# Kernel optimization log

Hardware: AMD Instinct MI355X
Metric: run time of the kernel (lower is better)

Reference implementation:

```python
import jax, jax.numpy as jnp
import numpy as np

N = 20000          # num nodes
E_EDGES = 160000   # num edges
D = 128            # input feature dim
H = 128            # hidden dim
C = 128            # num_classes (expert output dim)
NE = 4             # num_experts
COEF = 0.01        # load-balancing loss coefficient


def setup_inputs() -> dict:
    key = jax.random.key(0)
    ks = jax.random.split(key, 8)
    x = jax.random.normal(ks[0], (N, D), jnp.float32)
    edge_index = jax.random.randint(ks[1], (2, E_EDGES), 0, N)
    x_agg = jax.random.normal(ks[2], (N, D), jnp.float32)
    # gate params (w_gate is zeros-init in source; use small randn so gating is exercised)
    w_gate = jax.random.normal(ks[3], (D, NE), jnp.float32) * 0.1
    gate_threshold = jax.random.normal(ks[4], (NE,), jnp.float32) * 0.1
    experts_mask = jnp.ones((NE,), jnp.float32)
    # per-expert 2-layer GCN weights (vectorized over expert dim)
    W1 = jax.random.normal(ks[5], (NE, D, H), jnp.float32) * (1.0 / np.sqrt(D))
    b1 = jnp.zeros((NE, H), jnp.float32)
    W2 = jax.random.normal(ks[6], (NE, H, C), jnp.float32) * (1.0 / np.sqrt(H))
    b2 = jnp.zeros((NE, C), jnp.float32)
    return {"x": x, "edge_index": edge_index, "x_agg": x_agg,
            "w_gate": w_gate, "gate_threshold": gate_threshold,
            "experts_mask": experts_mask, "W1": W1, "b1": b1, "W2": W2, "b2": b2}


def _gcn_norm(edge_index):
    src, dst = edge_index[0], edge_index[1]
    deg = jax.ops.segment_sum(jnp.ones((src.shape[0],), jnp.float32), dst, num_segments=N)
    deg = jnp.maximum(deg, 1.0)
    norm = jax.lax.rsqrt(deg[src] * deg[dst])  # symmetric GCN normalization per edge
    return src, dst, norm


def _agg(h, src, dst, norm):
    # h: [N, F] -> normalized neighbor sum: [N, F]
    return jax.ops.segment_sum(h[src] * norm[:, None], dst, num_segments=N)


def _ste_sign(s):
    # SAGMMGateBackward: sign in forward, identity in backward (straight-through)
    return s + jax.lax.stop_gradient(jnp.sign(s) - s)


def reference(x, edge_index, x_agg, w_gate, gate_threshold, experts_mask, W1, b1, W2, b2):
    src, dst, norm = _gcn_norm(edge_index)

    # --- noisy_top_any gating (eval path: no noise), add_sigmoid=True ---
    clean_logits = x_agg @ w_gate                       # [N, NE]
    gate_scores = jax.nn.sigmoid(clean_logits)          # [N, NE]
    # sign-based straight-through gate vs learned threshold, masked by experts_mask
    gates = jax.nn.relu(_ste_sign(gate_scores - gate_threshold[None, :]))
    gates = gates * experts_mask[None, :]               # [N, NE], binary in forward

    # --- experts: 4 two-layer GCNs, vectorized over the expert dim ---
    agg_x = _agg(x, src, dst, norm)                     # shared first aggregation [N, D]
    h = jax.nn.relu(jnp.einsum('nd,edh->enh', agg_x, W1) + b1[:, None, :])   # [NE, N, H]
    agg_h = jax.vmap(lambda hh: _agg(hh, src, dst, norm))(h)                 # [NE, N, H]
    expert_out = jnp.einsum('enh,ehc->enc', agg_h, W2) + b2[:, None, :]      # [NE, N, C]

    # --- combine expert outputs with gates ---
    output = jnp.einsum('ne,enc->nc', gates, expert_out)                     # [N, C]

    # --- cv_squared load-balancing loss on per-expert importance ---
    importance = gates.sum(axis=0)                                           # [NE]
    load_loss = COEF * (jnp.var(importance) / (jnp.mean(importance) ** 2 + 1e-10))
    return output, load_loss
```

## Files before the change

### kernel.cpp

```cpp
#include <hip/hip_runtime.h>
#include <cstdint>
#include <cstddef>

#define NNODES 20000
#define NEDGES 160000
#define DFEAT  128
#define NEXP   4

typedef unsigned short u16;
typedef __attribute__((ext_vector_type(8))) short short8v;
typedef __attribute__((ext_vector_type(4))) float float4v;

static __device__ __forceinline__ u16 f2bf(float f) {
    union { float f; unsigned int i; } v; v.f = f;
    unsigned int r = (v.i + 0x7FFFu + ((v.i >> 16) & 1u)) >> 16;
    return (u16)r;
}
static __device__ __forceinline__ float lo2f(unsigned int u) { return __uint_as_float(u << 16); }
static __device__ __forceinline__ float hi2f(unsigned int u) { return __uint_as_float(u & 0xFFFF0000u); }


__global__ void k_pre(const int* __restrict__ ei,
                      const float* __restrict__ W1, const float* __restrict__ W2,
                      const float* __restrict__ x_agg, const float* __restrict__ w_gate,
                      const float* __restrict__ thr, const float* __restrict__ mask,
                      float* __restrict__ deg, u16* __restrict__ W1t, u16* __restrict__ W2t,
                      float* __restrict__ gates, float* __restrict__ importance) {
    int b = blockIdx.x;
    if (b < 625) {
        int e = b * 256 + threadIdx.x;
        if (e < NEDGES) atomicAdd(&deg[ei[NEDGES + e]], 1.0f);
        return;
    }
    if (b < 1137) {
        int gid = (b - 625) * 256 + threadIdx.x;
        int arr = gid >> 16;
        int rem = gid & 65535;
        int e = rem >> 14;
        int cw = rem & 16383;
        int c = cw >> 7, k = cw & 127;
        const float* W = arr ? W2 : W1;
        u16* Wt = arr ? W2t : W1t;
        Wt[rem] = f2bf(W[(size_t)e * 16384 + (size_t)k * 128 + c]);
        return;
    }
    int n = (b - 1137) * 256 + threadIdx.x;
    float4 lg = make_float4(0.f, 0.f, 0.f, 0.f);
    if (n < NNODES) {
        const float4* xr = (const float4*)(x_agg + (size_t)n * DFEAT);
        const float4* wg = (const float4*)w_gate;
        for (int k4 = 0; k4 < 32; ++k4) {
            float4 xv = xr[k4];
            float4 w0 = wg[4 * k4 + 0], w1 = wg[4 * k4 + 1];
            float4 w2 = wg[4 * k4 + 2], w3 = wg[4 * k4 + 3];
            lg.x += xv.x * w0.x + xv.y * w1.x + xv.z * w2.x + xv.w * w3.x;
            lg.y += xv.x * w0.y + xv.y * w1.y + xv.z * w2.y + xv.w * w3.y;
            lg.z += xv.x * w0.z + xv.y * w1.z + xv.z * w2.z + xv.w * w3.z;
            lg.w += xv.x * w0.w + xv.y * w1.w + xv.z * w2.w + xv.w * w3.w;
        }
    }
    float g[4];
    float lv[4] = {lg.x, lg.y, lg.z, lg.w};
    for (int e = 0; e < 4; ++e) {
        float sgm = 1.0f / (1.0f + expf(-lv[e]));
        g[e] = (sgm - thr[e] > 0.0f) ? mask[e] : 0.0f;
        if (n >= NNODES) g[e] = 0.0f;
    }
    if (n < NNODES) ((float4*)gates)[n] = make_float4(g[0], g[1], g[2], g[3]);
    int lane = threadIdx.x & 63;
    for (int e = 0; e < 4; ++e) {
        float v = g[e];
        for (int off = 32; off >= 1; off >>= 1) v += __shfl_down(v, off);
        if (lane == 0) atomicAdd(&importance[e], v);
    }
}

__global__ void k_scan(const float* __restrict__ deg, int* __restrict__ rowstart) {
    __shared__ int part[1024];
    int t = threadIdx.x;
    const int PER = 20;
    int base = t * PER;
    int s = 0;
    for (int i = 0; i < PER; ++i) {
        int n = base + i;
        if (n < NNODES) s += (int)deg[n];
    }
    part[t] = s;
    __syncthreads();
    for (int off = 1; off < 1024; off <<= 1) {
        int v = (t >= off) ? part[t - off] : 0;
        __syncthreads();
        part[t] += v;
        __syncthreads();
    }
    int run = part[t] - s;
    for (int i = 0; i < PER; ++i) {
        int n = base + i;
        if (n < NNODES) {
            rowstart[n] = run;
            run += (int)deg[n];
        }
    }
    if (t == 1023) rowstart[NNODES] = part[1023];
}

__global__ void k_fill(const int* __restrict__ ei, const float* __restrict__ deg,
                       const int* __restrict__ rowstart, int* __restrict__ cursor,
                       int* __restrict__ csrc, float* __restrict__ cnrm) {
    int e = blockIdx.x * 256 + threadIdx.x;
    if (e >= NEDGES) return;
    int s = ei[e], d = ei[NEDGES + e];
    int pos = atomicAdd(&cursor[d], 1);
    int slot = rowstart[d] + pos;
    csrc[slot] = s;
    float ds = fmaxf(deg[s], 1.0f), dd = fmaxf(deg[d], 1.0f);
    cnrm[slot] = 1.0f / sqrtf(ds * dd);
}

__global__ void k_aggx(const float* __restrict__ x, const int* __restrict__ rowstart,
                       const int* __restrict__ csrc, const float* __restrict__ cnrm,
                       u16* __restrict__ aggx) {
    int gid = blockIdx.x * 256 + threadIdx.x;
    if (gid >= NNODES * 32) return;
    int c4 = gid & 31, node = gid >> 5;
    int r0 = rowstart[node], r1 = rowstart[node + 1];
    float ax = 0.f, ay = 0.f, az = 0.f, aw = 0.f;
    for (int j = r0; j < r1; ++j) {
        int s = csrc[j];
        float wv = cnrm[j];
        float4 v = ((const float4*)(x + (size_t)s * DFEAT))[c4];
        ax += wv * v.x; ay += wv * v.y; az += wv * v.z; aw += wv * v.w;
    }
    uint2 o;
    o.x = ((unsigned)f2bf(ay) << 16) | f2bf(ax);
    o.y = ((unsigned)f2bf(aw) << 16) | f2bf(az);
    ((uint2*)(aggx + (size_t)node * DFEAT))[c4] = o;
}

__launch_bounds__(320)
__global__ void k_gemm1(const u16* __restrict__ aggx, const u16* __restrict__ W1t,
                        const float* __restrict__ b1, u16* __restrict__ h) {
    int e = blockIdx.y;
    int w = threadIdx.x >> 6, l = threadIdx.x & 63;
    int rbase = blockIdx.x * 80 + w * 16;
    int lr = l & 15, kg = l >> 4;

    const short8v* A8 = (const short8v*)aggx;
    const short8v* B8 = (const short8v*)(W1t + (size_t)e * 16384);

    short8v a[4];
#pragma unroll
    for (int kk = 0; kk < 4; ++kk) a[kk] = A8[(size_t)(rbase + lr) * 16 + kk * 4 + kg];

    u16* hb = h + (size_t)e * NNODES * DFEAT;
#pragma unroll
    for (int c = 0; c < 8; ++c) {
        float4v acc = {0.f, 0.f, 0.f, 0.f};
#pragma unroll
        for (int kk = 0; kk < 4; ++kk) {
            short8v b = B8[(c * 16 + lr) * 16 + kk * 4 + kg];
            acc = __builtin_amdgcn_mfma_f32_16x16x32_bf16(a[kk], b, acc, 0, 0, 0);
        }
        float bv = b1[e * DFEAT + c * 16 + lr];
#pragma unroll
        for (int i = 0; i < 4; ++i) {
            int node = rbase + kg * 4 + i;
            float vv = fmaxf(acc[i] + bv, 0.f);
            hb[(size_t)node * DFEAT + c * 16 + lr] = f2bf(vv);
        }
    }
}

__global__ void k_aggh(const u16* __restrict__ h, const int* __restrict__ rowstart,
                       const int* __restrict__ csrc, const float* __restrict__ cnrm,
                       const float* __restrict__ gates, u16* __restrict__ aggh) {
    int gid = blockIdx.x * 256 + threadIdx.x;
    if (gid >= NEXP * NNODES * 16) return;
    int l8 = gid & 15;
    int ni = gid >> 4;
    int node = ni % NNODES;
    int e = ni / NNODES;
    if (gates[(size_t)node * 4 + e] == 0.0f) return;
    const u16* hb = h + (size_t)e * NNODES * DFEAT;
    int r0 = rowstart[node], r1 = rowstart[node + 1];
    float a0 = 0.f, a1 = 0.f, a2 = 0.f, a3 = 0.f, a4 = 0.f, a5 = 0.f, a6 = 0.f, a7 = 0.f;
    for (int j = r0; j < r1; ++j) {
        int s = csrc[j];
        float wv = cnrm[j];
        uint4 v = ((const uint4*)(hb + (size_t)s * DFEAT))[l8];
        a0 += wv * lo2f(v.x); a1 += wv * hi2f(v.x);
        a2 += wv * lo2f(v.y); a3 += wv * hi2f(v.y);
        a4 += wv * lo2f(v.z); a5 += wv * hi2f(v.z);
        a6 += wv * lo2f(v.w); a7 += wv * hi2f(v.w);
    }
    uint4 o;
    o.x = ((unsigned)f2bf(a1) << 16) | f2bf(a0);
    o.y = ((unsigned)f2bf(a3) << 16) | f2bf(a2);
    o.z = ((unsigned)f2bf(a5) << 16) | f2bf(a4);
    o.w = ((unsigned)f2bf(a7) << 16) | f2bf(a6);
    ((uint4*)(aggh + (size_t)ni * DFEAT))[l8] = o;
}

__launch_bounds__(320)
__global__ void k_gemm2(const u16* __restrict__ aggh, const u16* __restrict__ W2t,
                        const float* __restrict__ b2, const float* __restrict__ gates,
                        const float* __restrict__ importance, float* __restrict__ out) {
    if (blockIdx.x == 0 && blockIdx.y == 0 && threadIdx.x == 0) {
        float v0 = importance[0], v1 = importance[1], v2 = importance[2], v3 = importance[3];
        float mean = 0.25f * (v0 + v1 + v2 + v3);
        float d0 = v0 - mean, d1 = v1 - mean, d2 = v2 - mean, d3 = v3 - mean;
        float var = 0.25f * (d0 * d0 + d1 * d1 + d2 * d2 + d3 * d3);
        out[(size_t)NNODES * DFEAT] = 0.01f * var / (mean * mean + 1e-10f);
    }
    int w = threadIdx.x >> 6, l = threadIdx.x & 63;
    int rbase = blockIdx.x * 80 + w * 16;
    int cb = blockIdx.y * 2;
    int lr = l & 15, kg = l >> 4;

    float4v acc[2];
    acc[0] = (float4v){0.f, 0.f, 0.f, 0.f};
    acc[1] = (float4v){0.f, 0.f, 0.f, 0.f};

#pragma unroll
    for (int e = 0; e < NEXP; ++e) {
        const short8v* A8 = (const short8v*)(aggh + (size_t)e * NNODES * DFEAT);
        const short8v* B8 = (const short8v*)(W2t + (size_t)e * 16384);
        short8v a[4];
#pragma unroll
        for (int kk = 0; kk < 4; ++kk) a[kk] = A8[(size_t)(rbase + lr) * 16 + kk * 4 + kg];
        float g[4];
#pragma unroll
        for (int i = 0; i < 4; ++i) g[i] = gates[(size_t)(rbase + kg * 4 + i) * 4 + e];
#pragma unroll
        for (int c = 0; c < 2; ++c) {
            float4v t = {0.f, 0.f, 0.f, 0.f};
#pragma unroll
            for (int kk = 0; kk < 4; ++kk) {
                short8v b = B8[((cb + c) * 16 + lr) * 16 + kk * 4 + kg];
                t = __builtin_amdgcn_mfma_f32_16x16x32_bf16(a[kk], b, t, 0, 0, 0);
            }
            float bv = b2[e * DFEAT + (cb + c) * 16 + lr];
#pragma unroll
            for (int i = 0; i < 4; ++i) acc[c][i] += g[i] * (t[i] + bv);
        }
    }

#pragma unroll
    for (int c = 0; c < 2; ++c)
#pragma unroll
        for (int i = 0; i < 4; ++i) {
            int node = rbase + kg * 4 + i;
            out[(size_t)node * DFEAT + (cb + c) * 16 + lr] = acc[c][i];
        }
}

extern "C" void kernel_launch(void* const* d_in, const int* in_sizes, int n_in,
                              void* d_out, int out_size, void* d_ws, size_t ws_size,
                              hipStream_t stream) {
    const float* x      = (const float*)d_in[0];
    const int*   ei     = (const int*)d_in[1];
    const float* x_agg  = (const float*)d_in[2];
    const float* w_gate = (const float*)d_in[3];
    const float* thr    = (const float*)d_in[4];
    const float* mask   = (const float*)d_in[5];
    const float* W1     = (const float*)d_in[6];
    const float* b1     = (const float*)d_in[7];
    const float* W2     = (const float*)d_in[8];
    const float* b2     = (const float*)d_in[9];
    float* out = (float*)d_out;
    float* ws  = (float*)d_ws;

    float* deg        = ws;
    int*   cursor     = (int*)(ws + 20000);
    float* importance = ws + 40000;
    int*   rowstart   = (int*)(ws + 40960);
    int*   csrc       = (int*)(ws + 61440);
    float* cnrm       = ws + 221440;
    float* gates      = ws + 381440;
    u16*   W1t        = (u16*)(ws + 461440);
    u16*   W2t        = (u16*)(ws + 494208);
    u16*   aggx       = (u16*)(ws + 526976);
    u16*   h          = (u16*)(ws + 1806976);
    u16*   aggh       = (u16*)(ws + 6926976);

    hipMemsetAsync(d_ws, 0, 40008 * sizeof(float), stream);

    k_pre<<<1216, 256, 0, stream>>>(ei, W1, W2, x_agg, w_gate, thr, mask,
                                    deg, W1t, W2t, gates, importance);
    k_scan<<<1, 1024, 0, stream>>>(deg, rowstart);
    k_fill<<<(NEDGES + 255) / 256, 256, 0, stream>>>(ei, deg, rowstart, cursor, csrc, cnrm);
    k_aggx<<<(NNODES * 32) / 256, 256, 0, stream>>>(x, rowstart, csrc, cnrm, aggx);
    k_gemm1<<<dim3(250, NEXP), 320, 0, stream>>>(aggx, W1t, b1, h);
    k_aggh<<<(NEXP * NNODES * 16) / 256, 256, 0, stream>>>(h, rowstart, csrc, cnrm, gates, aggh);
    k_gemm2<<<dim3(250, 4), 320, 0, stream>>>(aggh, W2t, b2, gates, importance, out);
}
```

Measured before the change: 258.8 us.

## Pre-convert x to bf16, unroll gather loops, tile weight transpose via LDS

Converts x to bf16 inside the preprocessing kernel so the first neighbor aggregation gathers half as many bytes per edge, with each thread handling 8 features instead of 4. Both aggregation kernels unroll the edge loop by four to keep more independent gathers in flight. The weight transpose now goes through a padded shared-memory tile so both its reads and writes are coalesced. This adds a full pass over x and extra workspace, and rounds x to bf16 before aggregation instead of after, which slightly changes numerics.

```diff
diff --git a/kernel.cpp b/kernel.cpp
--- a/kernel.cpp
+++ b/kernel.cpp
@@ -16,63 +16,98 @@
     unsigned int r = (v.i + 0x7FFFu + ((v.i >> 16) & 1u)) >> 16;
     return (u16)r;
 }
+static __device__ __forceinline__ unsigned pack2(float a, float b) {
+    return ((unsigned)f2bf(b) << 16) | f2bf(a);
+}
 static __device__ __forceinline__ float lo2f(unsigned int u) { return __uint_as_float(u << 16); }
 static __device__ __forceinline__ float hi2f(unsigned int u) { return __uint_as_float(u & 0xFFFF0000u); }
 
-
-__global__ void k_pre(const int* __restrict__ ei,
+static __device__ __forceinline__ void acc8(float w, uint4 v, float* a) {
+    a[0] += w * lo2f(v.x); a[1] += w * hi2f(v.x);
+    a[2] += w * lo2f(v.y); a[3] += w * hi2f(v.y);
+    a[4] += w * lo2f(v.z); a[5] += w * hi2f(v.z);
+    a[6] += w * lo2f(v.w); a[7] += w * hi2f(v.w);
+}
+
+
+__global__ void k_pre(const int* __restrict__ ei, const float* __restrict__ x,
                       const float* __restrict__ W1, const float* __restrict__ W2,
                       const float* __restrict__ x_agg, const float* __restrict__ w_gate,
                       const float* __restrict__ thr, const float* __restrict__ mask,
                       float* __restrict__ deg, u16* __restrict__ W1t, u16* __restrict__ W2t,
-                      float* __restrict__ gates, float* __restrict__ importance) {
+                      float* __restrict__ gates, float* __restrict__ importance,
+                      u16* __restrict__ xbf) {
     int b = blockIdx.x;
     if (b < 625) {
         int e = b * 256 + threadIdx.x;
         if (e < NEDGES) atomicAdd(&deg[ei[NEDGES + e]], 1.0f);
         return;
     }
-    if (b < 1137) {
-        int gid = (b - 625) * 256 + threadIdx.x;
-        int arr = gid >> 16;
-        int rem = gid & 65535;
-        int e = rem >> 14;
-        int cw = rem & 16383;
-        int c = cw >> 7, k = cw & 127;
+    if (b < 753) {
+        __shared__ u16 tile[32][33];
+        int tb = b - 625;
+        int arr = tb >> 6;
+        int t6 = tb & 63;
+        int e  = t6 >> 4;
+        int kt = (t6 >> 2) & 3;
+        int ct = t6 & 3;
         const float* W = arr ? W2 : W1;
         u16* Wt = arr ? W2t : W1t;
-        Wt[rem] = f2bf(W[(size_t)e * 16384 + (size_t)k * 128 + c]);
+        int ty = threadIdx.x >> 5, tx = threadIdx.x & 31;
+#pragma unroll
+        for (int r = 0; r < 4; ++r) {
+            int k = kt * 32 + ty + r * 8;
+            int c = ct * 32 + tx;
+            tile[ty + r * 8][tx] = f2bf(W[(size_t)e * 16384 + (size_t)k * 128 + c]);
+        }
+        __syncthreads();
+#pragma unroll
+        for (int r = 0; r < 4; ++r) {
+            int c = ct * 32 + ty + r * 8;
+            int k = kt * 32 + tx;
+            Wt[(size_t)e * 16384 + (size_t)c * 128 + k] = tile[tx][ty + r * 8];
+        }
         return;
     }
-    int n = (b - 1137) * 256 + threadIdx.x;
-    float4 lg = make_float4(0.f, 0.f, 0.f, 0.f);
-    if (n < NNODES) {
-        const float4* xr = (const float4*)(x_agg + (size_t)n * DFEAT);
-        const float4* wg = (const float4*)w_gate;
-        for (int k4 = 0; k4 < 32; ++k4) {
-            float4 xv = xr[k4];
-            float4 w0 = wg[4 * k4 + 0], w1 = wg[4 * k4 + 1];
-            float4 w2 = wg[4 * k4 + 2], w3 = wg[4 * k4 + 3];
-            lg.x += xv.x * w0.x + xv.y * w1.x + xv.z * w2.x + xv.w * w3.x;
-            lg.y += xv.x * w0.y + xv.y * w1.y + xv.z * w2.y + xv.w * w3.y;
-            lg.z += xv.x * w0.z + xv.y * w1.z + xv.z * w2.z + xv.w * w3.z;
-            lg.w += xv.x * w0.w + xv.y * w1.w + xv.z * w2.w + xv.w * w3.w;
-        }
-    }
-    float g[4];
-    float lv[4] = {lg.x, lg.y, lg.z, lg.w};
-    for (int e = 0; e < 4; ++e) {
-        float sgm = 1.0f / (1.0f + expf(-lv[e]));
-        g[e] = (sgm - thr[e] > 0.0f) ? mask[e] : 0.0f;
-        if (n >= NNODES) g[e] = 0.0f;
-    }
-    if (n < NNODES) ((float4*)gates)[n] = make_float4(g[0], g[1], g[2], g[3]);
-    int lane = threadIdx.x & 63;
-    for (int e = 0; e < 4; ++e) {
-        float v = g[e];
-        for (int off = 32; off >= 1; off >>= 1) v += __shfl_down(v, off);
-        if (lane == 0) atomicAdd(&importance[e], v);
-    }
+    if (b < 832) {
+        int n = (b - 753) * 256 + threadIdx.x;
+        float4 lg = make_float4(0.f, 0.f, 0.f, 0.f);
+        if (n < NNODES) {
+            const float4* xr = (const float4*)(x_agg + (size_t)n * DFEAT);
+            const float4* wg = (const float4*)w_gate;
+            for (int k4 = 0; k4 < 32; ++k4) {
+                float4 xv = xr[k4];
+                float4 w0 = wg[4 * k4 + 0], w1 = wg[4 * k4 + 1];
+                float4 w2 = wg[4 * k4 + 2], w3 = wg[4 * k4 + 3];
+                lg.x += xv.x * w0.x + xv.y * w1.x + xv.z * w2.x + xv.w * w3.x;
+                lg.y += xv.x * w0.y + xv.y * w1.y + xv.z * w2.y + xv.w * w3.y;
+                lg.z += xv.x * w0.z + xv.y * w1.z + xv.z * w2.z + xv.w * w3.z;
+                lg.w += xv.x * w0.w + xv.y * w1.w + xv.z * w2.w + xv.w * w3.w;
+            }
+        }
+        float g[4];
+        float lv[4] = {lg.x, lg.y, lg.z, lg.w};
+        for (int e = 0; e < 4; ++e) {
+            float sgm = 1.0f / (1.0f + expf(-lv[e]));
+            g[e] = (sgm - thr[e] > 0.0f) ? mask[e] : 0.0f;
+            if (n >= NNODES) g[e] = 0.0f;
+        }
+        if (n < NNODES) ((float4*)gates)[n] = make_float4(g[0], g[1], g[2], g[3]);
+        int lane = threadIdx.x & 63;
+        for (int e = 0; e < 4; ++e) {
+            float v = g[e];
+            for (int off = 32; off >= 1; off >>= 1) v += __shfl_down(v, off);
+            if (lane == 0) atomicAdd(&importance[e], v);
+        }
+        return;
+    }
+    int t8 = (b - 832) * 256 + threadIdx.x;
+    const float4* xr = (const float4*)x + (size_t)t8 * 2;
+    float4 v0 = xr[0], v1 = xr[1];
+    uint4 o;
+    o.x = pack2(v0.x, v0.y); o.y = pack2(v0.z, v0.w);
+    o.z = pack2(v1.x, v1.y); o.w = pack2(v1.z, v1.w);
+    ((uint4*)xbf)[t8] = o;
 }
 
 __global__ void k_scan(const float* __restrict__ deg, int* __restrict__ rowstart) {
@@ -117,24 +152,34 @@
     cnrm[slot] = 1.0f / sqrtf(ds * dd);
 }
 
-__global__ void k_aggx(const float* __restrict__ x, const int* __restrict__ rowstart,
+__global__ void k_aggx(const u16* __restrict__ xbf, const int* __restrict__ rowstart,
                        const int* __restrict__ csrc, const float* __restrict__ cnrm,
                        u16* __restrict__ aggx) {
     int gid = blockIdx.x * 256 + threadIdx.x;
-    if (gid >= NNODES * 32) return;
-    int c4 = gid & 31, node = gid >> 5;
+    if (gid >= NNODES * 16) return;
+    int l8 = gid & 15, node = gid >> 4;
     int r0 = rowstart[node], r1 = rowstart[node + 1];
-    float ax = 0.f, ay = 0.f, az = 0.f, aw = 0.f;
-    for (int j = r0; j < r1; ++j) {
+    float a[8] = {0.f, 0.f, 0.f, 0.f, 0.f, 0.f, 0.f, 0.f};
+    int j = r0;
+    for (; j + 4 <= r1; j += 4) {
+        int s0 = csrc[j], s1 = csrc[j + 1], s2 = csrc[j + 2], s3 = csrc[j + 3];
+        float w0 = cnrm[j], w1 = cnrm[j + 1], w2 = cnrm[j + 2], w3 = cnrm[j + 3];
+        uint4 v0 = ((const uint4*)(xbf + (size_t)s0 * DFEAT))[l8];
+        uint4 v1 = ((const uint4*)(xbf + (size_t)s1 * DFEAT))[l8];
+        uint4 v2 = ((const uint4*)(xbf + (size_t)s2 * DFEAT))[l8];
+        uint4 v3 = ((const uint4*)(xbf + (size_t)s3 * DFEAT))[l8];
+        acc8(w0, v0, a); acc8(w1, v1, a); acc8(w2, v2, a); acc8(w3, v3, a);
+    }
+    for (; j < r1; ++j) {
         int s = csrc[j];
-        float wv = cnrm[j];
-        float4 v = ((const float4*)(x + (size_t)s * DFEAT))[c4];
-        ax += wv * v.x; ay += wv * v.y; az += wv * v.z; aw += wv * v.w;
-    }
-    uint2 o;
-    o.x = ((unsigned)f2bf(ay) << 16) | f2bf(ax);
-    o.y = ((unsigned)f2bf(aw) << 16) | f2bf(az);
-    ((uint2*)(aggx + (size_t)node * DFEAT))[c4] = o;
+        float w = cnrm[j];
+        uint4 v = ((const uint4*)(xbf + (size_t)s * DFEAT))[l8];
+        acc8(w, v, a);
+    }
+    uint4 o;
+    o.x = pack2(a[0], a[1]); o.y = pack2(a[2], a[3]);
+    o.z = pack2(a[4], a[5]); o.w = pack2(a[6], a[7]);
+    ((uint4*)(aggx + (size_t)node * DFEAT))[l8] = o;
 }
 
 __launch_bounds__(320)
@@ -183,21 +228,26 @@
     if (gates[(size_t)node * 4 + e] == 0.0f) return;
     const u16* hb = h + (size_t)e * NNODES * DFEAT;
     int r0 = rowstart[node], r1 = rowstart[node + 1];
-    float a0 = 0.f, a1 = 0.f, a2 = 0.f, a3 = 0.f, a4 = 0.f, a5 = 0.f, a6 = 0.f, a7 = 0.f;
-    for (int j = r0; j < r1; ++j) {
+    float a[8] = {0.f, 0.f, 0.f, 0.f, 0.f, 0.f, 0.f, 0.f};
+    int j = r0;
+    for (; j + 4 <= r1; j += 4) {
+        int s0 = csrc[j], s1 = csrc[j + 1], s2 = csrc[j + 2], s3 = csrc[j + 3];
+        float w0 = cnrm[j], w1 = cnrm[j + 1], w2 = cnrm[j + 2], w3 = cnrm[j + 3];
+        uint4 v0 = ((const uint4*)(hb + (size_t)s0 * DFEAT))[l8];
+        uint4 v1 = ((const uint4*)(hb + (size_t)s1 * DFEAT))[l8];
+        uint4 v2 = ((const uint4*)(hb + (size_t)s2 * DFEAT))[l8];
+        uint4 v3 = ((const uint4*)(hb + (size_t)s3 * DFEAT))[l8];
+        acc8(w0, v0, a); acc8(w1, v1, a); acc8(w2, v2, a); acc8(w3, v3, a);
+    }
+    for (; j < r1; ++j) {
         int s = csrc[j];
-        float wv = cnrm[j];
+        float w = cnrm[j];
         uint4 v = ((const uint4*)(hb + (size_t)s * DFEAT))[l8];
-        a0 += wv * lo2f(v.x); a1 += wv * hi2f(v.x);
-        a2 += wv * lo2f(v.y); a3 += wv * hi2f(v.y);
-        a4 += wv * lo2f(v.z); a5 += wv * hi2f(v.z);
-        a6 += wv * lo2f(v.w); a7 += wv * hi2f(v.w);
+        acc8(w, v, a);
     }
     uint4 o;
-    o.x = ((unsigned)f2bf(a1) << 16) | f2bf(a0);
-    o.y = ((unsigned)f2bf(a3) << 16) | f2bf(a2);
-    o.z = ((unsigned)f2bf(a5) << 16) | f2bf(a4);
-    o.w = ((unsigned)f2bf(a7) << 16) | f2bf(a6);
+    o.x = pack2(a[0], a[1]); o.y = pack2(a[2], a[3]);
+    o.z = pack2(a[4], a[5]); o.w = pack2(a[6], a[7]);
     ((uint4*)(aggh + (size_t)ni * DFEAT))[l8] = o;
 }
 
@@ -279,17 +329,18 @@
     float* gates      = ws + 381440;
     u16*   W1t        = (u16*)(ws + 461440);
     u16*   W2t        = (u16*)(ws + 494208);
-    u16*   aggx       = (u16*)(ws + 526976);
-    u16*   h          = (u16*)(ws + 1806976);
-    u16*   aggh       = (u16*)(ws + 6926976);
+    u16*   xbf        = (u16*)(ws + 526976);
+    u16*   aggx       = (u16*)(ws + 1806976);
+    u16*   h          = (u16*)(ws + 3086976);
+    u16*   aggh       = (u16*)(ws + 8206976);
 
     hipMemsetAsync(d_ws, 0, 40008 * sizeof(float), stream);
 
-    k_pre<<<1216, 256, 0, stream>>>(ei, W1, W2, x_agg, w_gate, thr, mask,
-                                    deg, W1t, W2t, gates, importance);
+    k_pre<<<2082, 256, 0, stream>>>(ei, x, W1, W2, x_agg, w_gate, thr, mask,
+                                    deg, W1t, W2t, gates, importance, xbf);
     k_scan<<<1, 1024, 0, stream>>>(deg, rowstart);
     k_fill<<<(NEDGES + 255) / 256, 256, 0, stream>>>(ei, deg, rowstart, cursor, csrc, cnrm);
-    k_aggx<<<(NNODES * 32) / 256, 256, 0, stream>>>(x, rowstart, csrc, cnrm, aggx);
+    k_aggx<<<(NNODES * 16) / 256, 256, 0, stream>>>(xbf, rowstart, csrc, cnrm, aggx);
     k_gemm1<<<dim3(250, NEXP), 320, 0, stream>>>(aggx, W1t, b1, h);
     k_aggh<<<(NEXP * NNODES * 16) / 256, 256, 0, stream>>>(h, rowstart, csrc, cnrm, gates, aggh);
     k_gemm2<<<dim3(250, 4), 320, 0, stream>>>(aggh, W2t, b2, gates, importance, out);
```

Result: faster. 242.5 us (-6.3%).
